# Optimization experiments

Measured on AMD Instinct MI355X. Metric: run time of the kernel, lower is better.

## Reference

```python
import jax, jax.numpy as jnp
import numpy as np

W = 5      # window size
H = 4      # num heads (num_channels)
EPS = 1e-6

def rmsnorm(x, w):
    return x * w * jax.lax.rsqrt(jnp.mean(x * x, axis=-1, keepdims=True) + EPS)

def dwconv3d(x, k):
    # x: [B,D0,D1,D2,C], k: [3,3,3,1,C] depthwise 3x3x3 conv, SAME padding
    return jax.lax.conv_general_dilated(
        x, k, (1, 1, 1), 'SAME',
        dimension_numbers=('NDHWC', 'DHWIO', 'NDHWC'),
        feature_group_count=x.shape[-1])

def _part(t):
    # [B,D0,D1,D2,C] -> [B*nw, W^3, C] non-overlapping 3D windows
    B, D0, D1, D2, C = t.shape
    t = t.reshape(B, D0 // W, W, D1 // W, W, D2 // W, W, C)
    t = t.transpose(0, 1, 3, 5, 2, 4, 6, 7)
    return t.reshape(-1, W ** 3, C)

def _unpart(t, B, D0, D1, D2):
    C = t.shape[-1]
    t = t.reshape(B, D0 // W, D1 // W, D2 // W, W, W, W, C)
    t = t.transpose(0, 1, 4, 2, 5, 3, 6, 7)
    return t.reshape(B, D0, D1, D2, C)

def _pool01(t):
    # mean-pool poolable_dims=(0,1) by factor W -> coarse grid
    B, D0, D1, D2, C = t.shape
    return t.reshape(B, D0 // W, W, D1 // W, W, D2, C).mean(axis=(2, 4))

def _mha(q, k, v):
    # q,k,v: [N, L, C] -> [N, L, C] multi-head attention
    N, L, C = q.shape
    dh = C // H
    q = q.reshape(N, L, H, dh)
    k = k.reshape(N, L, H, dh)
    v = v.reshape(N, L, H, dh)
    s = jnp.einsum('nqhd,nkhd->nhqk', q, k) * (1.0 / np.sqrt(dh))
    p = jax.nn.softmax(s, axis=-1)
    return jnp.einsum('nhqk,nkhd->nqhd', p, v).reshape(N, L, C)

def _hier_attn(x, qkv_w, qkv_b, proj_w, proj_b, dw_pre, dw_post, lr_down, lr_up):
    B, D0, D1, D2, C = x.shape
    # conv_position='both': pre depthwise-conv positional term
    xin = x + dwconv3d(x, dw_pre)
    qkv = xin @ qkv_w + qkv_b                     # [B,D0,D1,D2,3C]
    q, k, v = jnp.split(qkv, 3, axis=-1)
    # fine scale: windowed local attention in W^3 blocks
    fine = _unpart(_mha(_part(q), _part(k), _part(v)), B, D0, D1, D2)
    # coarse scale: pool dims (0,1) by W, global attention over coarse tokens
    qc, kc, vc = _pool01(q), _pool01(k), _pool01(v)
    Nc = qc.shape[1] * qc.shape[2] * qc.shape[3]
    oc = _mha(qc.reshape(B, Nc, C), kc.reshape(B, Nc, C), vc.reshape(B, Nc, C))
    oc = oc.reshape(B, D0 // W, D1 // W, D2, C)
    oc = jnp.repeat(jnp.repeat(oc, W, axis=1), W, axis=2)   # upsample to full grid
    # lowrank hierarchical merge of coarse branch into fine branch
    merged = fine + (oc @ lr_down) @ lr_up
    out = merged @ proj_w + proj_b
    out = out + xin                               # attn_residual
    out = out + dwconv3d(out, dw_post)            # post conv position
    return out

def setup_inputs() -> dict:
    key = jax.random.key(0)
    ks = jax.random.split(key, 8)
    B, D0, D1, D2, C = 4, 40, 40, 20, 256
    rank = C // 4
    s = 0.02
    return {
        'x': jax.random.normal(ks[0], (B, D0, D1, D2, C), jnp.float32),
        'norm1_w': jnp.ones((C,), jnp.float32),
        'attn_norm_w': jnp.ones((C,), jnp.float32),
        'qkv_w': jax.random.normal(ks[1], (C, 3 * C), jnp.float32) * s,
        'qkv_b': jnp.zeros((3 * C,), jnp.float32),
        'proj_w': jax.random.normal(ks[2], (C, C), jnp.float32) * s,
        'proj_b': jnp.zeros((C,), jnp.float32),
        'dw_pre': jax.random.normal(ks[3], (3, 3, 3, 1, C), jnp.float32) * s,
        'dw_post': jax.random.normal(ks[4], (3, 3, 3, 1, C), jnp.float32) * s,
        'lr_down': jax.random.normal(ks[5], (C, rank), jnp.float32) * s,
        'lr_up': jax.random.normal(ks[6], (rank, C), jnp.float32) * s,
    }

def reference(x, norm1_w, attn_norm_w, qkv_w, qkv_b, proj_w, proj_b,
              dw_pre, dw_post, lr_down, lr_up) -> jnp.ndarray:
    # x = x + attn_norm(hier_attn(norm1(x)))   (dropout inactive in eval)
    a = _hier_attn(rmsnorm(x, norm1_w), qkv_w, qkv_b, proj_w, proj_b,
                   dw_pre, dw_post, lr_down, lr_up)
    return x + rmsnorm(a, attn_norm_w)
```

## Files before the change

kernel.cpp:

```cpp
#include <hip/hip_runtime.h>

#define D0c 40
#define D1c 40
#define D2c 20
#define NVOX 128000

typedef __attribute__((ext_vector_type(4))) float f4;
typedef __attribute__((ext_vector_type(8))) __bf16 bf8;
typedef __attribute__((ext_vector_type(8))) unsigned short u8s;

static __device__ __forceinline__ unsigned short f2bf(float f) {
  union { float f; unsigned int u; } v; v.f = f;
  unsigned int r = v.u + 0x7fffu + ((v.u >> 16) & 1u);
  return (unsigned short)(r >> 16);
}
static __device__ __forceinline__ float bf2f(unsigned short h) {
  union { unsigned int u; float f; } v; v.u = ((unsigned int)h) << 16;
  return v.f;
}

#define MFMA16(a, b, c) __builtin_amdgcn_mfma_f32_16x16x32_bf16((a), (b), (c), 0, 0, 0)

static __device__ __forceinline__ void gload16(const void* g, void* l) {
  __builtin_amdgcn_global_load_lds((const __attribute__((address_space(1))) unsigned int*)g,
                                   (__attribute__((address_space(3))) unsigned int*)l, 16, 0, 0);
}

__global__ __launch_bounds__(256) void k_prepw(const float* __restrict__ qkv_w,
                                               const float* __restrict__ proj_w,
                                               unsigned short* __restrict__ wq,
                                               unsigned short* __restrict__ wp) {
  int id = blockIdx.x * 256 + threadIdx.x;
  if (id < 768 * 256) {
    int kk = id & 31, row = (id >> 5) & 127, kc = (id >> 12) & 7, nt = id >> 15;
    int n = nt * 128 + row, k = kc * 32 + kk;
    wq[id] = f2bf(qkv_w[k * 768 + n]);
  } else {
    int j = id - 768 * 256;
    int m = j >> 8, k = j & 255;
    wp[j] = f2bf(proj_w[k * 256 + m]);
  }
}

__global__ __launch_bounds__(256) void k_rms1(const float* __restrict__ x,
                                              const float* __restrict__ w,
                                              unsigned short* __restrict__ xn) {
  int wv = threadIdx.x >> 6, ln = threadIdx.x & 63;
  int n = blockIdx.x * 4 + wv;
  f4 v = ((const f4*)(x + (size_t)n * 256))[ln];
  float ss = v.x * v.x + v.y * v.y + v.z * v.z + v.w * v.w;
#pragma unroll
  for (int m = 32; m >= 1; m >>= 1) ss += __shfl_xor(ss, m);
  float rs = rsqrtf(ss * (1.f / 256.f) + 1e-6f);
  f4 wv4 = ((const f4*)w)[ln];
  ushort4 o;
  o.x = f2bf(v.x * wv4.x * rs); o.y = f2bf(v.y * wv4.y * rs);
  o.z = f2bf(v.z * wv4.z * rs); o.w = f2bf(v.w * wv4.w * rs);
  ((ushort4*)(xn + (size_t)n * 256))[ln] = o;
}

__global__ __launch_bounds__(256) void k_convpre(const unsigned short* __restrict__ xn,
                                                 const float* __restrict__ dw,
                                                 unsigned short* __restrict__ xin) {
  __shared__ float wl[6912];
  for (int i = threadIdx.x; i < 6912; i += 256) wl[i] = dw[i];
  __syncthreads();
  int wv = threadIdx.x >> 6, ln = threadIdx.x & 63;
  int col = blockIdx.x * 4 + wv;
  int z1 = col % D1c; int t = col / D1c; int z0 = t % D0c; int b = t / D0c;
  int c0 = ln * 4;

  const unsigned short* base[9];
  bool val[9];
#pragma unroll
  for (int c = 0; c < 9; c++) {
    int dy = c / 3 - 1, dx = c % 3 - 1;
    int y0 = z0 + dy, y1 = z1 + dx;
    val[c] = ((unsigned)y0 < (unsigned)D0c) && ((unsigned)y1 < (unsigned)D1c);
    int yy0 = val[c] ? y0 : z0, yy1 = val[c] ? y1 : z1;
    base[c] = xn + ((size_t)((b * D0c + yy0) * D1c + yy1) * D2c) * 256 + c0;
  }
  f4 a0 = {0.f,0.f,0.f,0.f}, a1 = {0.f,0.f,0.f,0.f}, a2 = {0.f,0.f,0.f,0.f};
  ushort4 nxt[9];
#pragma unroll
  for (int c = 0; c < 9; c++) {
    ushort4 ld = {0, 0, 0, 0};
    if (val[c]) ld = *(const ushort4*)(base[c]);
    nxt[c] = ld;
  }
  unsigned short* op = xin + ((size_t)col * D2c) * 256 + c0;

  for (int z = 0; z < 20; z++) {
    f4 cf[9];
#pragma unroll
    for (int c = 0; c < 9; c++) {
      cf[c].x = bf2f(nxt[c].x); cf[c].y = bf2f(nxt[c].y);
      cf[c].z = bf2f(nxt[c].z); cf[c].w = bf2f(nxt[c].w);
    }
    int zn = (z < 19) ? (z + 1) : 19;
#pragma unroll
    for (int c = 0; c < 9; c++) {
      ushort4 ld = {0, 0, 0, 0};
      if (val[c]) ld = *(const ushort4*)(base[c] + (size_t)zn * 256);
      nxt[c] = ld;
    }
#pragma unroll
    for (int c = 0; c < 9; c++) {
      const f4 w0 = *(const f4*)&wl[(c * 3 + 0) * 256 + c0];
      const f4 w1 = *(const f4*)&wl[(c * 3 + 1) * 256 + c0];
      const f4 w2 = *(const f4*)&wl[(c * 3 + 2) * 256 + c0];
      a0.x += w2.x * cf[c].x; a0.y += w2.y * cf[c].y; a0.z += w2.z * cf[c].z; a0.w += w2.w * cf[c].w;
      a1.x += w1.x * cf[c].x; a1.y += w1.y * cf[c].y; a1.z += w1.z * cf[c].z; a1.w += w1.w * cf[c].w;
      a2.x += w0.x * cf[c].x; a2.y += w0.y * cf[c].y; a2.z += w0.z * cf[c].z; a2.w += w0.w * cf[c].w;
    }
    a1.x += cf[4].x; a1.y += cf[4].y; a1.z += cf[4].z; a1.w += cf[4].w;
    if (z >= 1) {
      ushort4 o;
      o.x = f2bf(a0.x); o.y = f2bf(a0.y); o.z = f2bf(a0.z); o.w = f2bf(a0.w);
      *(ushort4*)op = o;
      op += 256;
    }
    a0 = a1; a1 = a2; a2 = (f4){0.f,0.f,0.f,0.f};
  }
  {
    ushort4 o;
    o.x = f2bf(a0.x); o.y = f2bf(a0.y); o.z = f2bf(a0.z); o.w = f2bf(a0.w);
    *(ushort4*)op = o;
  }
}

__global__ __launch_bounds__(256) void k_gemm_qkv(const unsigned short* __restrict__ a_bf,
                                                  const unsigned short* __restrict__ wq2,
                                                  const float* __restrict__ bias,
                                                  unsigned short* __restrict__ out) {
  __shared__ unsigned short As[32768];
  __shared__ unsigned short Bs[8192];
  int m0 = blockIdx.x * 128;
  int tid = threadIdx.x;
  int w = tid >> 6, l = tid & 63;
  int wv = w, ln = l;
  int wr = wv >> 1, wc = wv & 1;
  int lrow = ln & 15, lg = ln >> 4;

  {
    const char* Ab = (const char*)(a_bf + (size_t)m0 * 256);
    int lrowoff = (l >> 2) * 512 + (l & 3) * 16;
#pragma unroll
    for (int c = 0; c < 16; c++) {
      int q = w * 16 + c;
      gload16(Ab + (q & 7) * 8192 + (q >> 3) * 64 + lrowoff,
              ((char*)As) + q * 1024);
    }
  }
  {
    const char* gB = (const char*)wq2;
#pragma unroll
    for (int c = 0; c < 2; c++) {
      int q = w * 2 + c;
      gload16(gB + q * 1024 + l * 16, ((char*)Bs) + q * 1024);
    }
  }

  int buf = 0;
  f4 acc[4][4];
  for (int nt = 0; nt < 6; nt++) {
    float bvv[4];
#pragma unroll
    for (int j = 0; j < 4; j++) bvv[j] = bias[nt * 128 + wc * 64 + j * 16 + lrow];
#pragma unroll
    for (int i = 0; i < 4; i++)
#pragma unroll
      for (int j = 0; j < 4; j++) acc[i][j] = {0.f, 0.f, 0.f, 0.f};

    for (int kc = 0; kc < 8; kc++) {
      int t = nt * 8 + kc;
      if (t + 1 < 48) {
        const char* gB = (const char*)wq2 + (size_t)(t + 1) * 8192;
        char* lB = ((char*)Bs) + (buf ^ 1) * 8192;
#pragma unroll
        for (int c = 0; c < 2; c++) {
          int q = w * 2 + c;
          gload16(gB + q * 1024 + l * 16, lB + q * 1024);
        }
        asm volatile("s_waitcnt vmcnt(2)\n\ts_barrier" ::: "memory");
      } else {
        asm volatile("s_waitcnt vmcnt(0)\n\ts_barrier" ::: "memory");
      }
      bf8 af[4], bf_[4];
#pragma unroll
      for (int i = 0; i < 4; i++)
        af[i] = *(const bf8*)&As[kc * 4096 + (wr * 64 + i * 16 + lrow) * 32 + lg * 8];
#pragma unroll
      for (int j = 0; j < 4; j++)
        bf_[j] = *(const bf8*)&Bs[buf * 4096 + (wc * 64 + j * 16 + lrow) * 32 + lg * 8];
#pragma unroll
      for (int i = 0; i < 4; i++)
#pragma unroll
        for (int j = 0; j < 4; j++) acc[i][j] = MFMA16(af[i], bf_[j], acc[i][j]);
      asm volatile("s_barrier" ::: "memory");
      buf ^= 1;
    }
#pragma unroll
    for (int j = 0; j < 4; j++) {
      int col = nt * 128 + wc * 64 + j * 16 + lrow;
#pragma unroll
      for (int i = 0; i < 4; i++) {
        int row = m0 + wr * 64 + i * 16 + lg * 4;
#pragma unroll
        for (int r = 0; r < 4; r++)
          out[(size_t)(row + r) * 768 + col] = f2bf(acc[i][j][r] + bvv[j]);
      }
    }
  }
}

__global__ __launch_bounds__(256) void k_fineattn(const unsigned short* __restrict__ qkv,
                                                  unsigned short* __restrict__ fine) {
  __shared__ unsigned short sm[27136];
  unsigned short* Qs = sm;
  unsigned short* Ks = sm + 9216;
  unsigned short* Vt = sm + 18432;
  unsigned short* Ps = sm;
  int h = blockIdx.x & 3, wid = blockIdx.x >> 2;
  int w2 = wid & 3, w1 = (wid >> 2) & 7, w0 = (wid >> 5) & 7, b = wid >> 8;
  int tid = threadIdx.x;
  int tok = tid >> 1, half = tid & 1;
  if (tok < 125) {
    int i0 = tok / 25, rr = tok % 25, i1 = rr / 5, i2 = rr % 5;
    int n = ((b * D0c + w0 * 5 + i0) * D1c + w1 * 5 + i1) * D2c + w2 * 5 + i2;
    const u8s* qp = (const u8s*)(qkv + (size_t)n * 768 + h * 64 + half * 32);
    const u8s* kp = (const u8s*)(qkv + (size_t)n * 768 + 256 + h * 64 + half * 32);
    const unsigned short* vp = qkv + (size_t)n * 768 + 512 + h * 64 + half * 32;
#pragma unroll
    for (int e = 0; e < 4; e++) {
      *(u8s*)&Qs[tok * 72 + half * 32 + e * 8] = qp[e];
      *(u8s*)&Ks[tok * 72 + half * 32 + e * 8] = kp[e];
    }
#pragma unroll
    for (int d = 0; d < 32; d++) Vt[(half * 32 + d) * 136 + tok] = vp[d];
  } else {
    u8s z = {0, 0, 0, 0, 0, 0, 0, 0};
#pragma unroll
    for (int e = 0; e < 4; e++) {
      *(u8s*)&Qs[tok * 72 + half * 32 + e * 8] = z;
      *(u8s*)&Ks[tok * 72 + half * 32 + e * 8] = z;
    }
#pragma unroll
    for (int d = 0; d < 32; d++) Vt[(half * 32 + d) * 136 + tok] = 0;
  }
  __syncthreads();
  int wv = tid >> 6, ln = tid & 63, lrow = ln & 15, lg = ln >> 4;
  f4 s[2][8];
#pragma unroll
  for (int mi = 0; mi < 2; mi++)
#pragma unroll
    for (int ni = 0; ni < 8; ni++) s[mi][ni] = {0.f, 0.f, 0.f, 0.f};
  bf8 aq[2][2];
#pragma unroll
  for (int ks = 0; ks < 2; ks++)
#pragma unroll
    for (int mi = 0; mi < 2; mi++)
      aq[mi][ks] = *(const bf8*)&Qs[(wv * 32 + mi * 16 + lrow) * 72 + ks * 32 + lg * 8];
#pragma unroll
  for (int ni = 0; ni < 8; ni++) {
#pragma unroll
    for (int ks = 0; ks < 2; ks++) {
      bf8 bk = *(const bf8*)&Ks[(ni * 16 + lrow) * 72 + ks * 32 + lg * 8];
      s[0][ni] = MFMA16(aq[0][ks], bk, s[0][ni]);
      s[1][ni] = MFMA16(aq[1][ks], bk, s[1][ni]);
    }
  }
#pragma unroll
  for (int mi = 0; mi < 2; mi++) {
#pragma unroll
    for (int j = 0; j < 4; j++) {
      float mx = -3e38f;
#pragma unroll
      for (int ni = 0; ni < 8; ni++) {
        int col = ni * 16 + lrow;
        float v = (col < 125) ? s[mi][ni][j] * 0.125f : -3e38f;
        s[mi][ni][j] = v;
        mx = fmaxf(mx, v);
      }
#pragma unroll
      for (int m = 8; m >= 1; m >>= 1) mx = fmaxf(mx, __shfl_xor(mx, m));
      float sum = 0.f;
#pragma unroll
      for (int ni = 0; ni < 8; ni++) {
        float p = __expf(s[mi][ni][j] - mx);
        s[mi][ni][j] = p;
        sum += p;
      }
#pragma unroll
      for (int m = 8; m >= 1; m >>= 1) sum += __shfl_xor(sum, m);
      float inv = 1.f / sum;
#pragma unroll
      for (int ni = 0; ni < 8; ni++) s[mi][ni][j] *= inv;
    }
  }
  __syncthreads();
#pragma unroll
  for (int mi = 0; mi < 2; mi++)
#pragma unroll
    for (int ni = 0; ni < 8; ni++)
#pragma unroll
      for (int j = 0; j < 4; j++)
        Ps[(wv * 32 + mi * 16 + lg * 4 + j) * 136 + ni * 16 + lrow] = f2bf(s[mi][ni][j]);
  __syncthreads();
  f4 o[2][4];
#pragma unroll
  for (int mi = 0; mi < 2; mi++)
#pragma unroll
    for (int ni = 0; ni < 4; ni++) o[mi][ni] = {0.f, 0.f, 0.f, 0.f};
#pragma unroll
  for (int ks = 0; ks < 4; ks++) {
    bf8 ap0 = *(const bf8*)&Ps[(wv * 32 + 0 + lrow) * 136 + ks * 32 + lg * 8];
    bf8 ap1 = *(const bf8*)&Ps[(wv * 32 + 16 + lrow) * 136 + ks * 32 + lg * 8];
#pragma unroll
    for (int ni = 0; ni < 4; ni++) {
      bf8 bv = *(const bf8*)&Vt[(ni * 16 + lrow) * 136 + ks * 32 + lg * 8];
      o[0][ni] = MFMA16(ap0, bv, o[0][ni]);
      o[1][ni] = MFMA16(ap1, bv, o[1][ni]);
    }
  }
#pragma unroll
  for (int mi = 0; mi < 2; mi++) {
    int rt0 = wv * 32 + mi * 16 + lg * 4;
#pragma unroll
    for (int r = 0; r < 4; r++) {
      int tk = rt0 + r;
      if (tk >= 125) continue;
      int i0 = tk / 25, rr = tk % 25, i1 = rr / 5, i2 = rr % 5;
      int n = ((b * D0c + w0 * 5 + i0) * D1c + w1 * 5 + i1) * D2c + w2 * 5 + i2;
#pragma unroll
      for (int ni = 0; ni < 4; ni++)
        fine[(size_t)n * 256 + h * 64 + ni * 16 + lrow] = f2bf(o[mi][ni][r]);
    }
  }
}

__global__ __launch_bounds__(256) void k_pool(const unsigned short* __restrict__ qkv,
                                              unsigned short* __restrict__ qc,
                                              unsigned short* __restrict__ kc,
                                              unsigned short* __restrict__ vct) {
  int ct = blockIdx.x;
  int z2 = ct % 20; int t = ct / 20; int c1 = t & 7; int c0 = (t >> 3) & 7; int b = t >> 6;
  int tid = threadIdx.x;
  float a0 = 0.f, a1 = 0.f, a2 = 0.f;
  for (int i0 = 0; i0 < 5; i0++)
    for (int i1 = 0; i1 < 5; i1++) {
      int n = ((b * D0c + c0 * 5 + i0) * D1c + c1 * 5 + i1) * D2c + z2;
      const unsigned short* row = qkv + (size_t)n * 768;
      a0 += bf2f(row[tid]);
      a1 += bf2f(row[tid + 256]);
      a2 += bf2f(row[tid + 512]);
    }
  const float sc = 1.f / 25.f;
  qc[(size_t)ct * 256 + tid] = f2bf(a0 * sc);
  kc[(size_t)ct * 256 + tid] = f2bf(a1 * sc);
  int h = tid >> 6, d = tid & 63;
  int tk = ct - b * 1280;
  vct[(((size_t)b * 4 + h) * 64 + d) * 1288 + tk] = f2bf(a2 * sc);
}

__global__ __launch_bounds__(256) void k_coarse(const unsigned short* __restrict__ qc,
                                                const unsigned short* __restrict__ kc,
                                                const unsigned short* __restrict__ vct,
                                                float* __restrict__ oc) {
  __shared__ unsigned short Qs[9216];
  __shared__ unsigned short KP[9216];
  __shared__ unsigned short Vts[4608];
  int qt = blockIdx.x;
  int b = blockIdx.y >> 2, h = blockIdx.y & 3;
  int tid = threadIdx.x, wv = tid >> 6, ln = tid & 63, lrow = ln & 15, lg = ln >> 4;
  {
    int tk = tid >> 1, half = tid & 1;
    const u8s* qp = (const u8s*)(qc + (size_t)(b * 1280 + qt * 128 + tk) * 256 + h * 64 + half * 32);
#pragma unroll
    for (int e = 0; e < 4; e++) *(u8s*)&Qs[tk * 72 + half * 32 + e * 8] = qp[e];
  }
  float mrun[2][4], srun[2][4];
  f4 o[2][4];
#pragma unroll
  for (int mi = 0; mi < 2; mi++)
#pragma unroll
    for (int j = 0; j < 4; j++) { mrun[mi][j] = -3e38f; srun[mi][j] = 0.f; }
#pragma unroll
  for (int mi = 0; mi < 2; mi++)
#pragma unroll
    for (int ni = 0; ni < 4; ni++) o[mi][ni] = {0.f, 0.f, 0.f, 0.f};

  int ktok = tid >> 2, kq = (tid & 3) * 16;
  int vd = tid >> 2, vtc = (tid & 3) * 16;

  for (int kt = 0; kt < 20; kt++) {
    {
      const u8s* kp = (const u8s*)(kc + (size_t)(b * 1280 + kt * 64 + ktok) * 256 + h * 64 + kq);
      *(u8s*)&KP[ktok * 72 + kq] = kp[0];
      *(u8s*)&KP[ktok * 72 + kq + 8] = kp[1];
      const u8s* vp = (const u8s*)(vct + (((size_t)b * 4 + h) * 64 + vd) * 1288 + kt * 64 + vtc);
      *(u8s*)&Vts[vd * 72 + vtc] = vp[0];
      *(u8s*)&Vts[vd * 72 + vtc + 8] = vp[1];
    }
    __syncthreads();
    f4 s[2][4];
#pragma unroll
    for (int mi = 0; mi < 2; mi++)
#pragma unroll
      for (int ni = 0; ni < 4; ni++) s[mi][ni] = {0.f, 0.f, 0.f, 0.f};
    bf8 aq[2][2];
#pragma unroll
    for (int ks = 0; ks < 2; ks++)
#pragma unroll
      for (int mi = 0; mi < 2; mi++)
        aq[mi][ks] = *(const bf8*)&Qs[(wv * 32 + mi * 16 + lrow) * 72 + ks * 32 + lg * 8];
#pragma unroll
    for (int ni = 0; ni < 4; ni++) {
#pragma unroll
      for (int ks = 0; ks < 2; ks++) {
        bf8 bk = *(const bf8*)&KP[(ni * 16 + lrow) * 72 + ks * 32 + lg * 8];
        s[0][ni] = MFMA16(aq[0][ks], bk, s[0][ni]);
        s[1][ni] = MFMA16(aq[1][ks], bk, s[1][ni]);
      }
    }
#pragma unroll
    for (int mi = 0; mi < 2; mi++) {
#pragma unroll
      for (int j = 0; j < 4; j++) {
        float mx = -3e38f;
#pragma unroll
        for (int ni = 0; ni < 4; ni++) {
          float v = s[mi][ni][j] * 0.125f;
          s[mi][ni][j] = v;
          mx = fmaxf(mx, v);
        }
#pragma unroll
        for (int m = 8; m >= 1; m >>= 1) mx = fmaxf(mx, __shfl_xor(mx, m));
        float nm = fmaxf(mrun[mi][j], mx);
        float alpha = __expf(mrun[mi][j] - nm);
        mrun[mi][j] = nm;
        float sum = 0.f;
#pragma unroll
        for (int ni = 0; ni < 4; ni++) {
          float p = __expf(s[mi][ni][j] - nm);
          s[mi][ni][j] = p;
          sum += p;
        }
#pragma unroll
        for (int m = 8; m >= 1; m >>= 1) sum += __shfl_xor(sum, m);
        srun[mi][j] = srun[mi][j] * alpha + sum;
#pragma unroll
        for (int ni = 0; ni < 4; ni++) o[mi][ni][j] *= alpha;
      }
    }
    __syncthreads();
#pragma unroll
    for (int mi = 0; mi < 2; mi++)
#pragma unroll
      for (int ni = 0; ni < 4; ni++)
#pragma unroll
        for (int j = 0; j < 4; j++)
          KP[(wv * 32 + mi * 16 + lg * 4 + j) * 72 + ni * 16 + lrow] = f2bf(s[mi][ni][j]);
    __syncthreads();
#pragma unroll
    for (int ks = 0; ks < 2; ks++) {
      bf8 ap0 = *(const bf8*)&KP[(wv * 32 + 0 + lrow) * 72 + ks * 32 + lg * 8];
      bf8 ap1 = *(const bf8*)&KP[(wv * 32 + 16 + lrow) * 72 + ks * 32 + lg * 8];
#pragma unroll
      for (int ni = 0; ni < 4; ni++) {
        bf8 bv = *(const bf8*)&Vts[(ni * 16 + lrow) * 72 + ks * 32 + lg * 8];
        o[0][ni] = MFMA16(ap0, bv, o[0][ni]);
        o[1][ni] = MFMA16(ap1, bv, o[1][ni]);
      }
    }
    __syncthreads();
  }
#pragma unroll
  for (int mi = 0; mi < 2; mi++)
#pragma unroll
    for (int j = 0; j < 4; j++) {
      float inv = 1.f / srun[mi][j];
      int row = qt * 128 + wv * 32 + mi * 16 + lg * 4 + j;
      float* orow = oc + ((size_t)(b * 1280 + row)) * 256 + h * 64;
#pragma unroll
      for (int ni = 0; ni < 4; ni++) orow[ni * 16 + lrow] = o[mi][ni][j] * inv;
    }
}

__global__ __launch_bounds__(256) void k_lowrank(const float* __restrict__ oc,
                                                 const float* __restrict__ lrd,
                                                 const float* __restrict__ lru,
                                                 float* __restrict__ oclr) {
  __shared__ float tmp[16 * 64];
  int t0 = blockIdx.x * 16;
  int tid = threadIdx.x;
  int i = tid >> 4, r4 = (tid & 15) * 4;
  f4 a = {0.f, 0.f, 0.f, 0.f};
  const float* orow = oc + (size_t)(t0 + i) * 256;
  for (int k = 0; k < 256; k++) {
    float ov = orow[k];
    const f4 w = *(const f4*)&lrd[k * 64 + r4];
    a.x += ov * w.x; a.y += ov * w.y; a.z += ov * w.z; a.w += ov * w.w;
  }
  *(f4*)&tmp[i * 64 + r4] = a;
  __syncthreads();
  int c16 = (tid & 15) * 16;
  f4 acc0 = {0.f,0.f,0.f,0.f}, acc1 = {0.f,0.f,0.f,0.f}, acc2 = {0.f,0.f,0.f,0.f}, acc3 = {0.f,0.f,0.f,0.f};
  for (int r = 0; r < 64; r++) {
    float tv = tmp[i * 64 + r];
    const f4* wr = (const f4*)&lru[r * 256 + c16];
    f4 w0 = wr[0], w1 = wr[1], w2 = wr[2], w3 = wr[3];
    acc0.x += tv * w0.x; acc0.y += tv * w0.y; acc0.z += tv * w0.z; acc0.w += tv * w0.w;
    acc1.x += tv * w1.x; acc1.y += tv * w1.y; acc1.z += tv * w1.z; acc1.w += tv * w1.w;
    acc2.x += tv * w2.x; acc2.y += tv * w2.y; acc2.z += tv * w2.z; acc2.w += tv * w2.w;
    acc3.x += tv * w3.x; acc3.y += tv * w3.y; acc3.z += tv * w3.z; acc3.w += tv * w3.w;
  }
  float* outr = oclr + (size_t)(t0 + i) * 256 + c16;
  *(f4*)&outr[0] = acc0; *(f4*)&outr[4] = acc1; *(f4*)&outr[8] = acc2; *(f4*)&outr[12] = acc3;
}

__global__ __launch_bounds__(256) void k_gemm_proj(const unsigned short* __restrict__ fine,
                                                   const float* __restrict__ oclr,
                                                   const unsigned short* __restrict__ wt,
                                                   const float* __restrict__ bias,
                                                   const unsigned short* __restrict__ xin,
                                                   unsigned short* __restrict__ out1) {
  __shared__ unsigned short As[128 * 40];
  __shared__ unsigned short Bs[128 * 40];
  int m0 = blockIdx.y * 128, n0 = blockIdx.x * 128;
  int tid = threadIdx.x;
  int wv = tid >> 6, ln = tid & 63;
  int wr = wv >> 1, wc = wv & 1;
  int lrow = ln & 15, lg = ln >> 4;
  f4 acc[4][4];
#pragma unroll
  for (int i = 0; i < 4; i++)
#pragma unroll
    for (int j = 0; j < 4; j++) acc[i][j] = {0.f, 0.f, 0.f, 0.f};
  int srow = tid >> 1, sk = (tid & 1) * 16;
  int nrow = m0 + srow;
  int z2 = nrow % D2c; int tt = nrow / D2c; int z1 = tt % D1c; tt /= D1c; int z0 = tt % D0c; int bb = tt / D0c;
  int ct = ((bb * 8 + z0 / 5) * 8 + z1 / 5) * 20 + z2;
  for (int k0 = 0; k0 < 256; k0 += 32) {
    const unsigned short* fp = fine + (size_t)nrow * 256 + k0 + sk;
    const float* cp = oclr + (size_t)ct * 256 + k0 + sk;
    u8s f0 = *(const u8s*)fp, f1 = *(const u8s*)(fp + 8);
    u8s t0, t1;
#pragma unroll
    for (int e = 0; e < 8; e++) {
      t0[e] = f2bf(bf2f(f0[e]) + cp[e]);
      t1[e] = f2bf(bf2f(f1[e]) + cp[8 + e]);
    }
    *(u8s*)&As[srow * 40 + sk] = t0;
    *(u8s*)&As[srow * 40 + sk + 8] = t1;
    const u8s* bp = (const u8s*)(wt + (size_t)(n0 + srow) * 256 + k0 + sk);
    *(u8s*)&Bs[srow * 40 + sk] = bp[0];
    *(u8s*)&Bs[srow * 40 + sk + 8] = bp[1];
    __syncthreads();
    bf8 af[4], bf_[4];
#pragma unroll
    for (int i = 0; i < 4; i++) af[i] = *(const bf8*)&As[(wr * 64 + i * 16 + lrow) * 40 + lg * 8];
#pragma unroll
    for (int j = 0; j < 4; j++) bf_[j] = *(const bf8*)&Bs[(wc * 64 + j * 16 + lrow) * 40 + lg * 8];
#pragma unroll
    for (int i = 0; i < 4; i++)
#pragma unroll
      for (int j = 0; j < 4; j++) acc[i][j] = MFMA16(af[i], bf_[j], acc[i][j]);
    __syncthreads();
  }
#pragma unroll
  for (int j = 0; j < 4; j++) {
    int col = n0 + wc * 64 + j * 16 + lrow;
    float bv = bias[col];
#pragma unroll
    for (int i = 0; i < 4; i++) {
      int row = m0 + wr * 64 + i * 16 + lg * 4;
#pragma unroll
      for (int r = 0; r < 4; r++) {
        float xr = bf2f(xin[(size_t)(row + r) * 256 + col]);
        out1[(size_t)(row + r) * 256 + col] = f2bf(acc[i][j][r] + bv + xr);
      }
    }
  }
}

__global__ __launch_bounds__(256) void k_convpost(const unsigned short* __restrict__ o1,
                                                  const float* __restrict__ dw,
                                                  const float* __restrict__ x,
                                                  const float* __restrict__ anw,
                                                  float* __restrict__ outp) {
  __shared__ float wl[6912];
  for (int i = threadIdx.x; i < 6912; i += 256) wl[i] = dw[i];
  __syncthreads();
  int wv = threadIdx.x >> 6, ln = threadIdx.x & 63;
  int col = blockIdx.x * 4 + wv;
  int z1 = col % D1c; int t = col / D1c; int z0 = t % D0c; int b = t / D0c;
  int c0 = ln * 4;

  const unsigned short* base[9];
  bool val[9];
#pragma unroll
  for (int c = 0; c < 9; c++) {
    int dy = c / 3 - 1, dx = c % 3 - 1;
    int y0 = z0 + dy, y1 = z1 + dx;
    val[c] = ((unsigned)y0 < (unsigned)D0c) && ((unsigned)y1 < (unsigned)D1c);
    int yy0 = val[c] ? y0 : z0, yy1 = val[c] ? y1 : z1;
    base[c] = o1 + ((size_t)((b * D0c + yy0) * D1c + yy1) * D2c) * 256 + c0;
  }
  f4 a0 = {0.f,0.f,0.f,0.f}, a1 = {0.f,0.f,0.f,0.f}, a2 = {0.f,0.f,0.f,0.f};
  ushort4 nxt[9];
#pragma unroll
  for (int c = 0; c < 9; c++) {
    ushort4 ld = {0, 0, 0, 0};
    if (val[c]) ld = *(const ushort4*)(base[c]);
    nxt[c] = ld;
  }
  const f4 wv4 = *(const f4*)(anw + c0);
  const float* xp = x + ((size_t)col * D2c) * 256 + c0;
  float* op = outp + ((size_t)col * D2c) * 256 + c0;

  for (int z = 0; z < 20; z++) {
    f4 cf[9];
#pragma unroll
    for (int c = 0; c < 9; c++) {
      cf[c].x = bf2f(nxt[c].x); cf[c].y = bf2f(nxt[c].y);
      cf[c].z = bf2f(nxt[c].z); cf[c].w = bf2f(nxt[c].w);
    }
    int zn = (z < 19) ? (z + 1) : 19;
#pragma unroll
    for (int c = 0; c < 9; c++) {
      ushort4 ld = {0, 0, 0, 0};
      if (val[c]) ld = *(const ushort4*)(base[c] + (size_t)zn * 256);
      nxt[c] = ld;
    }
#pragma unroll
    for (int c = 0; c < 9; c++) {
      const f4 w0 = *(const f4*)&wl[(c * 3 + 0) * 256 + c0];
      const f4 w1 = *(const f4*)&wl[(c * 3 + 1) * 256 + c0];
      const f4 w2 = *(const f4*)&wl[(c * 3 + 2) * 256 + c0];
      a0.x += w2.x * cf[c].x; a0.y += w2.y * cf[c].y; a0.z += w2.z * cf[c].z; a0.w += w2.w * cf[c].w;
      a1.x += w1.x * cf[c].x; a1.y += w1.y * cf[c].y; a1.z += w1.z * cf[c].z; a1.w += w1.w * cf[c].w;
      a2.x += w0.x * cf[c].x; a2.y += w0.y * cf[c].y; a2.z += w0.z * cf[c].z; a2.w += w0.w * cf[c].w;
    }
    a1.x += cf[4].x; a1.y += cf[4].y; a1.z += cf[4].z; a1.w += cf[4].w;
    if (z >= 1) {
      float ss = a0.x * a0.x + a0.y * a0.y + a0.z * a0.z + a0.w * a0.w;
#pragma unroll
      for (int m = 32; m >= 1; m >>= 1) ss += __shfl_xor(ss, m);
      float rs = rsqrtf(ss * (1.f / 256.f) + 1e-6f);
      f4 xv = *(const f4*)xp;
      f4 res;
      res.x = xv.x + a0.x * wv4.x * rs;
      res.y = xv.y + a0.y * wv4.y * rs;
      res.z = xv.z + a0.z * wv4.z * rs;
      res.w = xv.w + a0.w * wv4.w * rs;
      *(f4*)op = res;
      xp += 256; op += 256;
    }
    a0 = a1; a1 = a2; a2 = (f4){0.f,0.f,0.f,0.f};
  }
  {
    float ss = a0.x * a0.x + a0.y * a0.y + a0.z * a0.z + a0.w * a0.w;
#pragma unroll
    for (int m = 32; m >= 1; m >>= 1) ss += __shfl_xor(ss, m);
    float rs = rsqrtf(ss * (1.f / 256.f) + 1e-6f);
    f4 xv = *(const f4*)xp;
    f4 res;
    res.x = xv.x + a0.x * wv4.x * rs;
    res.y = xv.y + a0.y * wv4.y * rs;
    res.z = xv.z + a0.z * wv4.z * rs;
    res.w = xv.w + a0.w * wv4.w * rs;
    *(f4*)op = res;
  }
}

extern "C" void kernel_launch(void* const* d_in, const int* in_sizes, int n_in,
                              void* d_out, int out_size, void* d_ws, size_t ws_size,
                              hipStream_t stream) {
  const float* x          = (const float*)d_in[0];
  const float* norm1_w    = (const float*)d_in[1];
  const float* attn_norm_w= (const float*)d_in[2];
  const float* qkv_w      = (const float*)d_in[3];
  const float* qkv_b      = (const float*)d_in[4];
  const float* proj_w     = (const float*)d_in[5];
  const float* proj_b     = (const float*)d_in[6];
  const float* dw_pre     = (const float*)d_in[7];
  const float* dw_post    = (const float*)d_in[8];
  const float* lr_down    = (const float*)d_in[9];
  const float* lr_up      = (const float*)d_in[10];
  float* outp = (float*)d_out;

  unsigned char* w = (unsigned char*)d_ws;
  size_t off = 0;
  unsigned short* xn   = (unsigned short*)(w + off); off += 65536000ULL;
  unsigned short* xin  = (unsigned short*)(w + off); off += 65536000ULL;
  unsigned short* qkv  = (unsigned short*)(w + off); off += 196608000ULL;
  unsigned short* out1 = (unsigned short*)(w + off); off += 65536000ULL;
  unsigned short* qc   = (unsigned short*)(w + off); off += 2621440ULL;
  unsigned short* kc   = (unsigned short*)(w + off); off += 2621440ULL;
  unsigned short* vct  = (unsigned short*)(w + off); off += 2637824ULL;
  float* oc            = (float*)(w + off);          off += 5242880ULL;
  float* oclr          = (float*)(w + off);          off += 5242880ULL;
  unsigned short* wq   = (unsigned short*)(w + off); off += 393216ULL;
  unsigned short* wp   = (unsigned short*)(w + off); off += 131072ULL;
  unsigned short* fine = xn;

  k_prepw<<<1024, 256, 0, stream>>>(qkv_w, proj_w, wq, wp);
  k_rms1<<<32000, 256, 0, stream>>>(x, norm1_w, xn);
  k_convpre<<<1600, 256, 0, stream>>>(xn, dw_pre, xin);
  k_gemm_qkv<<<1000, 256, 0, stream>>>(xin, wq, qkv_b, qkv);
  k_fineattn<<<4096, 256, 0, stream>>>(qkv, fine);
  k_pool<<<5120, 256, 0, stream>>>(qkv, qc, kc, vct);
  k_coarse<<<dim3(10, 16), 256, 0, stream>>>(qc, kc, vct, oc);
  k_lowrank<<<320, 256, 0, stream>>>(oc, lr_down, lr_up, oclr);
  k_gemm_proj<<<dim3(2, 1000), 256, 0, stream>>>(fine, oclr, wp, proj_b, xin, out1);
  k_convpost<<<1600, 256, 0, stream>>>(out1, dw_post, x, attn_norm_w, outp);
}
```

Baseline: 716.3 us.

## Halve QKV GEMM row tile, swizzle LDS layout, stage output through LDS

The QKV projection GEMM now uses a 64-row tile instead of 128, doubling the grid to 2000 blocks and halving A-tile LDS so more blocks can be resident. The LDS layouts of A and B are XOR-swizzled; the weight prep kernel bakes the matching permutation into the bf16 weights. This is meant to cut bank conflicts on the MFMA operand reads. Output is staged through the idle B buffer in LDS and written as 16-byte row-contiguous stores instead of scattered 2-byte stores, at the cost of extra barriers and more B reloads per output row.

```diff
diff --git a/kernel.cpp b/kernel.cpp
--- a/kernel.cpp
+++ b/kernel.cpp
@@ -33,7 +33,10 @@
   int id = blockIdx.x * 256 + threadIdx.x;
   if (id < 768 * 256) {
     int kk = id & 31, row = (id >> 5) & 127, kc = (id >> 12) & 7, nt = id >> 15;
-    int n = nt * 128 + row, k = kc * 32 + kk;
+    int s = kk >> 3, kj = kk & 7;
+    int g = s ^ ((row >> 1) & 3);
+    int k = kc * 32 + g * 8 + kj;
+    int n = nt * 128 + row;
     wq[id] = f2bf(qkv_w[k * 768 + n]);
   } else {
     int j = id - 768 * 256;
@@ -133,42 +136,39 @@
                                                   const unsigned short* __restrict__ wq2,
                                                   const float* __restrict__ bias,
                                                   unsigned short* __restrict__ out) {
-  __shared__ unsigned short As[32768];
+  __shared__ unsigned short As[16384];
   __shared__ unsigned short Bs[8192];
-  int m0 = blockIdx.x * 128;
+  int m0 = blockIdx.x * 64;
   int tid = threadIdx.x;
   int w = tid >> 6, l = tid & 63;
-  int wv = w, ln = l;
-  int wr = wv >> 1, wc = wv & 1;
-  int lrow = ln & 15, lg = ln >> 4;
+  int wr = w >> 1, wc = w & 1;
+  int lrow = l & 15, lg = l >> 4;
 
   {
     const char* Ab = (const char*)(a_bf + (size_t)m0 * 256);
-    int lrowoff = (l >> 2) * 512 + (l & 3) * 16;
-#pragma unroll
-    for (int c = 0; c < 16; c++) {
-      int q = w * 16 + c;
-      gload16(Ab + (q & 7) * 8192 + (q >> 3) * 64 + lrowoff,
-              ((char*)As) + q * 1024);
-    }
+    int row = tid >> 2, s = tid & 3;
+    int g = s ^ ((row >> 1) & 3);
+    const char* src0 = Ab + row * 512 + g * 16;
+    char* dst0 = ((char*)As) + w * 1024 + l * 16;
+#pragma unroll
+    for (int kc = 0; kc < 8; kc++)
+      gload16(src0 + kc * 64, dst0 + kc * 4096);
   }
   {
     const char* gB = (const char*)wq2;
-#pragma unroll
-    for (int c = 0; c < 2; c++) {
-      int q = w * 2 + c;
-      gload16(gB + q * 1024 + l * 16, ((char*)Bs) + q * 1024);
-    }
+    char* lB = (char*)Bs;
+    gload16(gB + tid * 16, lB + w * 1024 + l * 16);
+    gload16(gB + 4096 + tid * 16, lB + 4096 + w * 1024 + l * 16);
   }
 
   int buf = 0;
-  f4 acc[4][4];
+  f4 acc[2][4];
   for (int nt = 0; nt < 6; nt++) {
     float bvv[4];
 #pragma unroll
     for (int j = 0; j < 4; j++) bvv[j] = bias[nt * 128 + wc * 64 + j * 16 + lrow];
 #pragma unroll
-    for (int i = 0; i < 4; i++)
+    for (int i = 0; i < 2; i++)
 #pragma unroll
       for (int j = 0; j < 4; j++) acc[i][j] = {0.f, 0.f, 0.f, 0.f};
 
@@ -177,39 +177,54 @@
       if (t + 1 < 48) {
         const char* gB = (const char*)wq2 + (size_t)(t + 1) * 8192;
         char* lB = ((char*)Bs) + (buf ^ 1) * 8192;
-#pragma unroll
-        for (int c = 0; c < 2; c++) {
-          int q = w * 2 + c;
-          gload16(gB + q * 1024 + l * 16, lB + q * 1024);
-        }
+        gload16(gB + tid * 16, lB + w * 1024 + l * 16);
+        gload16(gB + 4096 + tid * 16, lB + 4096 + w * 1024 + l * 16);
         asm volatile("s_waitcnt vmcnt(2)\n\ts_barrier" ::: "memory");
       } else {
         asm volatile("s_waitcnt vmcnt(0)\n\ts_barrier" ::: "memory");
       }
-      bf8 af[4], bf_[4];
-#pragma unroll
-      for (int i = 0; i < 4; i++)
-        af[i] = *(const bf8*)&As[kc * 4096 + (wr * 64 + i * 16 + lrow) * 32 + lg * 8];
-#pragma unroll
-      for (int j = 0; j < 4; j++)
-        bf_[j] = *(const bf8*)&Bs[buf * 4096 + (wc * 64 + j * 16 + lrow) * 32 + lg * 8];
-#pragma unroll
-      for (int i = 0; i < 4; i++)
+      bf8 af[2], bf_[4];
+#pragma unroll
+      for (int i = 0; i < 2; i++) {
+        int row = wr * 32 + i * 16 + lrow;
+        af[i] = *(const bf8*)&As[kc * 2048 + row * 32 + ((lg ^ ((row >> 1) & 3)) * 8)];
+      }
+#pragma unroll
+      for (int j = 0; j < 4; j++) {
+        int rowb = wc * 64 + j * 16 + lrow;
+        bf_[j] = *(const bf8*)&Bs[buf * 4096 + rowb * 32 + ((lg ^ ((rowb >> 1) & 3)) * 8)];
+      }
+#pragma unroll
+      for (int i = 0; i < 2; i++)
 #pragma unroll
         for (int j = 0; j < 4; j++) acc[i][j] = MFMA16(af[i], bf_[j], acc[i][j]);
       asm volatile("s_barrier" ::: "memory");
       buf ^= 1;
     }
-#pragma unroll
-    for (int j = 0; j < 4; j++) {
-      int col = nt * 128 + wc * 64 + j * 16 + lrow;
-#pragma unroll
-      for (int i = 0; i < 4; i++) {
-        int row = m0 + wr * 64 + i * 16 + lg * 4;
-#pragma unroll
-        for (int r = 0; r < 4; r++)
-          out[(size_t)(row + r) * 768 + col] = f2bf(acc[i][j][r] + bvv[j]);
-      }
+
+    unsigned short* Cs = &Bs[(buf ^ 1) * 4096];
+    int crow = tid >> 3, cseg = tid & 7;
+#pragma unroll
+    for (int h = 0; h < 2; h++) {
+      if (wr == h) {
+#pragma unroll
+        for (int i = 0; i < 2; i++)
+#pragma unroll
+          for (int j = 0; j < 4; j++)
+#pragma unroll
+            for (int r = 0; r < 4; r++)
+              Cs[(i * 16 + lg * 4 + r) * 128 + wc * 64 + j * 16 + lrow] =
+                  f2bf(acc[i][j][r] + bvv[j]);
+      }
+      asm volatile("s_waitcnt lgkmcnt(0)\n\ts_barrier" ::: "memory");
+      {
+        u8s v0 = *(const u8s*)&Cs[crow * 128 + cseg * 16];
+        u8s v1 = *(const u8s*)&Cs[crow * 128 + cseg * 16 + 8];
+        unsigned short* orow = out + (size_t)(m0 + h * 32 + crow) * 768 + nt * 128 + cseg * 16;
+        *(u8s*)orow = v0;
+        *(u8s*)(orow + 8) = v1;
+      }
+      asm volatile("s_waitcnt lgkmcnt(0)\n\ts_barrier" ::: "memory");
     }
   }
 }
@@ -708,7 +723,7 @@
   k_prepw<<<1024, 256, 0, stream>>>(qkv_w, proj_w, wq, wp);
   k_rms1<<<32000, 256, 0, stream>>>(x, norm1_w, xn);
   k_convpre<<<1600, 256, 0, stream>>>(xn, dw_pre, xin);
-  k_gemm_qkv<<<1000, 256, 0, stream>>>(xin, wq, qkv_b, qkv);
+  k_gemm_qkv<<<2000, 256, 0, stream>>>(xin, wq, qkv_b, qkv);
   k_fineattn<<<4096, 256, 0, stream>>>(qkv, fine);
   k_pool<<<5120, 256, 0, stream>>>(qkv, qc, kc, vct);
   k_coarse<<<dim3(10, 16), 256, 0, stream>>>(qc, kc, vct, oc);
```

Result: faster. 682.4 us (-4.7%).
